# Kernel tuning notes

Measured on AMD Instinct MI355X. Metric: run time of the kernel, lower is better.

## Reference

```python
import jax, jax.numpy as jnp
import numpy as np

N = 50000
IN_CH = 128
OUT_CH = 64
H1, C1 = 8, 8


def gat_layer(x, src, dst, W, att_src, att_dst, bias, heads, out_ch, concat, n_nodes):
    # x: [N, F_in]; W: [F_in, heads*out_ch]; att_*: [heads, out_ch]; bias: [heads*out_ch] or [out_ch]
    h = (x @ W).reshape(n_nodes, heads, out_ch)              # [N,H,C]
    a_src = jnp.einsum('nhc,hc->nh', h, att_src)             # [N,H]
    a_dst = jnp.einsum('nhc,hc->nh', h, att_dst)             # [N,H]
    e = jax.nn.leaky_relu(a_src[src] + a_dst[dst], 0.2)      # [E,H]
    # segment softmax over incoming edges of each dst node
    m = jax.ops.segment_max(e, dst, num_segments=n_nodes)    # [N,H]
    p = jnp.exp(e - m[dst])                                  # [E,H]
    s = jax.ops.segment_sum(p, dst, num_segments=n_nodes)    # [N,H]
    alpha = p / (s[dst] + 1e-16)                             # [E,H]
    out = jax.ops.segment_sum(h[src] * alpha[:, :, None], dst, num_segments=n_nodes)  # [N,H,C]
    out = out.reshape(n_nodes, heads * out_ch) if concat else out.mean(axis=1)
    return out + bias


def setup_inputs() -> dict:
    key = jax.random.key(0)
    ks = jax.random.split(key, 12)
    E = 1600000
    x = jax.random.normal(ks[0], (N, IN_CH), dtype=jnp.float32)
    edge_index = jax.random.randint(ks[1], (2, E), 0, N, dtype=jnp.int64)
    sc = 0.1
    return {
        'x': x,
        'edge_index': edge_index,
        'W1': jax.random.normal(ks[2], (IN_CH, H1 * C1), dtype=jnp.float32) * sc,
        'att_src1': jax.random.normal(ks[3], (H1, C1), dtype=jnp.float32) * sc,
        'att_dst1': jax.random.normal(ks[4], (H1, C1), dtype=jnp.float32) * sc,
        'b1': jnp.zeros((H1 * C1,), dtype=jnp.float32),
        'W2': jax.random.normal(ks[5], (H1 * C1, OUT_CH), dtype=jnp.float32) * sc,
        'att_src2': jax.random.normal(ks[6], (1, OUT_CH), dtype=jnp.float32) * sc,
        'att_dst2': jax.random.normal(ks[7], (1, OUT_CH), dtype=jnp.float32) * sc,
        'b2': jnp.zeros((OUT_CH,), dtype=jnp.float32),
        'lin_W': jax.random.normal(ks[8], (OUT_CH, 1), dtype=jnp.float32) * sc,
        'lin_b': jnp.zeros((1,), dtype=jnp.float32),
    }


def reference(x, edge_index, W1, att_src1, att_dst1, b1, W2, att_src2, att_dst2, b2, lin_W, lin_b):
    # add self loops (PyG GATConv default)
    loops = jnp.arange(N, dtype=edge_index.dtype)
    src = jnp.concatenate([edge_index[0], loops])
    dst = jnp.concatenate([edge_index[1], loops])
    # dropout layers are identity in eval mode
    h = gat_layer(x, src, dst, W1, att_src1, att_dst1, b1, H1, C1, True, N)
    h = jax.nn.elu(h)
    h = gat_layer(h, src, dst, W2, att_src2, att_dst2, b2, 1, OUT_CH, False, N)
    return h @ lin_W + lin_b
```

## Files before the change

### kernel.cpp

```cpp
#include <hip/hip_runtime.h>
#include <hip/hip_bf16.h>
#include <math.h>

#define NN     50000
#define FIN    128
#define F1     64
#define NH1    8
#define F2     64

#define BSH    256
#define NB     ((NN + BSH - 1) / BSH)
#define BCAP   9472

typedef __bf16 bf16x8 __attribute__((ext_vector_type(8)));
typedef float  f32x4  __attribute__((ext_vector_type(4)));


__device__ __forceinline__ float loadF(const void* p, long long i, int fp32) {
    if (fp32) return ((const float*)p)[i];
    return __bfloat162float(((const __hip_bfloat16*)p)[i]);
}
__device__ __forceinline__ int loadI_nt(const void* p, long long i, int i64) {
    if (i64) return (int)__builtin_nontemporal_load(&((const long long*)p)[i]);
    return __builtin_nontemporal_load(&((const int*)p)[i]);
}
__device__ __forceinline__ unsigned short f2bfu(float f) {
    unsigned u = __float_as_uint(f);
    return (unsigned short)((u + 0x7FFFu + ((u >> 16) & 1u)) >> 16);
}
__device__ __forceinline__ float b2f(unsigned short u) {
    return __uint_as_float(((unsigned)u) << 16);
}


#define PREB 49

__global__ __launch_bounds__(256) void k_pre(
    const void* __restrict__ x, const void* __restrict__ ei,
    int* __restrict__ flags,
    const void* __restrict__ W1, const void* __restrict__ W2,
    unsigned short* __restrict__ W1p, unsigned short* __restrict__ W2p,
    int* __restrict__ bcnt) {
    __shared__ int s_nanexp, s_oddnz, s_fp32;
    if (threadIdx.x == 0) { s_nanexp = 0; s_oddnz = 0; }
    if (blockIdx.x == 0 && threadIdx.x < NB) bcnt[threadIdx.x] = 0;
    __syncthreads();
    const unsigned short* u = (const unsigned short*)x;
    int cnt = 0;
    for (int i = threadIdx.x; i < 8192; i += 256) {
        unsigned short v = u[i];
        if ((v & 0x7F80) == 0x7F80) cnt++;
    }
    if (cnt) atomicAdd(&s_nanexp, cnt);
    const unsigned* e32 = (const unsigned*)ei;
    int nz = 0;
    for (int i = threadIdx.x; i < 2048; i += 256) {
        if (e32[2 * i + 1] != 0u) nz++;
    }
    if (nz) atomicAdd(&s_oddnz, nz);
    __syncthreads();
    if (threadIdx.x == 0) {
        s_fp32 = (s_nanexp > 2) ? 1 : 0;
        if (blockIdx.x == 0) {
            flags[0] = s_fp32;
            flags[1] = (s_oddnz == 0) ? 1 : 0;
        }
    }
    __syncthreads();
    int fp32 = s_fp32;
    int gt = blockIdx.x * 256 + threadIdx.x, gs = PREB * 256;
    for (int i = gt; i < (FIN / 32) * 4 * 512; i += gs) {
        int j = i & 7, l = (i >> 3) & 63, f = i >> 9;
        int kb = f >> 2, nt = f & 3;
        int k = kb * 32 + (l >> 4) * 8 + j, n = nt * 16 + (l & 15);
        W1p[i] = f2bfu(loadF(W1, k * 64 + n, fp32));
    }
    for (int i = gt; i < (F1 / 32) * 4 * 512; i += gs) {
        int j = i & 7, l = (i >> 3) & 63, f = i >> 9;
        int kb = f >> 2, nt = f & 3;
        int k = kb * 32 + (l >> 4) * 8 + j, n = nt * 16 + (l & 15);
        W2p[i] = f2bfu(loadF(W2, k * 64 + n, fp32));
    }
}


__global__ __launch_bounds__(1024) void k_bin_fine(
    const void* __restrict__ ei, int E, int Etot,
    int* __restrict__ bcnt, unsigned* __restrict__ binned,
    const int* __restrict__ flags) {
    int i64 = flags[1];
    __shared__ int hist[NB], gbase[NB];
    for (int i = threadIdx.x; i < NB; i += 1024) hist[i] = 0;
    __syncthreads();
    long long base = (long long)blockIdx.x * 8192;
    unsigned pk[8]; short bb[8];
    #pragma unroll
    for (int u = 0; u < 8; ++u) {
        long long j = base + u * 1024 + threadIdx.x;
        int s = -1, d = -1;
        if (j < Etot) {
            if (j < E) { s = loadI_nt(ei, j, i64); d = loadI_nt(ei, (long long)E + j, i64); }
            else       { s = d = (int)(j - E); }
        }
        if ((unsigned)s < NN && (unsigned)d < NN) {
            bb[u] = (short)(d >> 8);
            pk[u] = ((unsigned)s << 8) | (unsigned)(d & 255);
            atomicAdd(&hist[bb[u]], 1);
        } else bb[u] = -1;
    }
    __syncthreads();
    for (int i = threadIdx.x; i < NB; i += 1024) {
        int h = hist[i];
        gbase[i] = h ? atomicAdd(&bcnt[i], h) : 0;
        hist[i] = 0;
    }
    __syncthreads();
    #pragma unroll
    for (int u = 0; u < 8; ++u) {
        if (bb[u] >= 0) {
            int pos = gbase[bb[u]] + atomicAdd(&hist[bb[u]], 1);
            if (pos < BCAP) binned[(size_t)bb[u] * BCAP + pos] = pk[u];
        }
    }
}

__global__ __launch_bounds__(1024) void k_csr_local(
    const int* __restrict__ bcnt, const unsigned* __restrict__ binned,
    int* __restrict__ offs, int* __restrict__ perm) {
    __shared__ int hist[BSH], cur[BSH], sd[BSH];
    int bk = blockIdx.x, tid = threadIdx.x;
    int n0 = bk * BSH;
    if (tid < 256) sd[tid] = (tid < NB) ? min(bcnt[tid], BCAP) : 0;
    __syncthreads();
    for (int off = 1; off < BSH; off <<= 1) {
        int t = 0;
        if (tid < 256 && tid >= off) t = sd[tid - off];
        __syncthreads();
        if (tid < 256) sd[tid] += t;
        __syncthreads();
    }
    int gb = (bk > 0) ? sd[bk - 1] : 0;
    if (bk == 0 && tid == 0) offs[NN] = sd[NB - 1];
    __syncthreads();
    int cnt = bcnt[bk]; if (cnt > BCAP) cnt = BCAP;
    const unsigned* bp = binned + (size_t)bk * BCAP;
    if (tid < 256) hist[tid] = 0;
    __syncthreads();
    for (int i = tid; i < cnt; i += 1024)
        atomicAdd(&hist[bp[i] & 255], 1);
    __syncthreads();
    int myh = (tid < 256) ? hist[tid] : 0;
    if (tid < 256) sd[tid] = myh;
    __syncthreads();
    for (int off = 1; off < BSH; off <<= 1) {
        int t = 0;
        if (tid < 256 && tid >= off) t = sd[tid - off];
        __syncthreads();
        if (tid < 256) sd[tid] += t;
        __syncthreads();
    }
    if (tid < 256) {
        int excl = sd[tid] - myh;
        cur[tid] = gb + excl;
        if (n0 + tid < NN) offs[n0 + tid] = gb + excl;
    }
    __syncthreads();
    for (int i = tid; i < cnt; i += 1024) {
        unsigned pk = bp[i];
        int pos = atomicAdd(&cur[pk & 255], 1);
        perm[pos] = (int)(pk >> 8);
    }
}


__global__ __launch_bounds__(256) void k_mgemm1(
    const void* __restrict__ x, const unsigned short* __restrict__ W1p,
    const void* __restrict__ attS, const void* __restrict__ attD,
    __hip_bfloat16* __restrict__ h1, float* __restrict__ a1s,
    float* __restrict__ a1d, const int* __restrict__ flags) {
    int fp32 = flags[0];
    __shared__ unsigned short hl[64 * 64];
    __shared__ float attSl[64], attDl[64];
    int tid = threadIdx.x;
    if (tid < 64) { attSl[tid] = loadF(attS, tid, fp32); attDl[tid] = loadF(attD, tid, fp32); }
    int w = tid >> 6, l = tid & 63;
    int quad = l >> 4, lm = l & 15;
    int n0 = blockIdx.x * 64;

    bf16x8 bfr[16];
    #pragma unroll
    for (int f = 0; f < 16; ++f)
        bfr[f] = *(const bf16x8*)(W1p + f * 512 + l * 8);

    int nodeA = n0 + w * 16 + lm;
    long long rowA = (nodeA < NN) ? nodeA : 0;
    f32x4 acc[4];
    #pragma unroll
    for (int nt = 0; nt < 4; ++nt) acc[nt] = (f32x4){0.f, 0.f, 0.f, 0.f};

    #pragma unroll
    for (int kb = 0; kb < 4; ++kb) {
        bf16x8 af;
        if (!fp32) {
            af = *(const bf16x8*)((const unsigned short*)x + rowA * FIN + kb * 32 + quad * 8);
        } else {
            const float* xf = (const float*)x + rowA * FIN + kb * 32 + quad * 8;
            union { unsigned short s[8]; bf16x8 v; } tmp;
            #pragma unroll
            for (int j = 0; j < 8; ++j) tmp.s[j] = f2bfu(xf[j]);
            af = tmp.v;
        }
        #pragma unroll
        for (int nt = 0; nt < 4; ++nt)
            acc[nt] = __builtin_amdgcn_mfma_f32_16x16x32_bf16(af, bfr[kb * 4 + nt], acc[nt], 0, 0, 0);
    }

    #pragma unroll
    for (int nt = 0; nt < 4; ++nt) {
        #pragma unroll
        for (int r = 0; r < 4; ++r) {
            int nl = w * 16 + quad * 4 + r;
            int node = n0 + nl;
            int c = nt * 16 + lm;
            unsigned short hb = f2bfu(acc[nt][r]);
            hl[nl * 64 + c] = hb;
            if (node < NN) ((unsigned short*)h1)[(size_t)node * 64 + c] = hb;
        }
    }
    __syncthreads();
    #pragma unroll
    for (int pp = 0; pp < 2; ++pp) {
        int p = tid + pp * 256;
        int nl = p >> 3, g = p & 7;
        int node = n0 + nl;
        float ss = 0.f, dd = 0.f;
        #pragma unroll
        for (int j = 0; j < 8; ++j) {
            float hv = b2f(hl[nl * 64 + g * 8 + j]);
            ss += hv * attSl[g * 8 + j];
            dd += hv * attDl[g * 8 + j];
        }
        if (node < NN) {
            a1s[(size_t)node * NH1 + g] = ss;
            a1d[(size_t)node * NH1 + g] = dd;
        }
    }
}


#define HLP 72

__global__ __launch_bounds__(256) void k_agg1f(
    const int* __restrict__ offs, const int* __restrict__ perm,
    const __hip_bfloat16* __restrict__ h1, const float* __restrict__ a1s,
    const float* __restrict__ a1d, const void* __restrict__ b1,
    const unsigned short* __restrict__ W2p,
    const void* __restrict__ attS2, const void* __restrict__ attD2,
    __hip_bfloat16* __restrict__ h2, float* __restrict__ a2s,
    float* __restrict__ a2d, int n, const int* __restrict__ flags) {
    int fp32 = flags[0];
    __shared__ unsigned short hl[16 * HLP];
    __shared__ float attSl[64], attDl[64];
    __shared__ float sp[16 * 4], dp[16 * 4];
    int tid = threadIdx.x;
    if (tid < 64) { attSl[tid] = loadF(attS2, tid, fp32); attDl[tid] = loadF(attD2, tid, fp32); }
    int w = tid >> 6, c = tid & 63;
    int n0 = blockIdx.x * 16;
    int u = c & 7, h = c >> 3, cb = c & 56;
    const unsigned short* hu = (const unsigned short*)h1;

    for (int m = 0; m < 4; ++m) {
        int d = n0 + w * 4 + m;
        if (d < n) {
            int start = offs[d], end = offs[d + 1];
            float adl = a1d[(size_t)d * NH1 + h];
            float acc = 0.f, denp = 0.f;
            for (int i = start; i < end; i += 8) {
                int j = i + u;
                int jc = (j < end) ? j : (end - 1);
                int sj = perm[jc];
                float e = a1s[(size_t)sj * NH1 + h] + adl;
                e = fmaxf(e, 0.2f * e);
                float p = (j < end) ? __expf(e) : 0.f;
                denp += p;
                #pragma unroll
                for (int k = 0; k < 8; ++k) {
                    int su = __builtin_amdgcn_readlane(sj, k);
                    float pk = __shfl(p, cb + k, 64);
                    acc = fmaf(pk, b2f(hu[(size_t)su * 64 + c]), acc);
                }
            }
            denp += __shfl_xor(denp, 1, 64);
            denp += __shfl_xor(denp, 2, 64);
            denp += __shfl_xor(denp, 4, 64);
            float v = acc / (denp + 1e-16f) + loadF(b1, c, fp32);
            v = (v > 0.f) ? v : expm1f(v);
            hl[(w * 4 + m) * HLP + c] = f2bfu(v);
        }
    }
    __syncthreads();

    int quad = c >> 4, lm = c & 15;
    bf16x8 bf0 = *(const bf16x8*)(W2p + (0 * 4 + w) * 512 + c * 8);
    bf16x8 bf1 = *(const bf16x8*)(W2p + (1 * 4 + w) * 512 + c * 8);
    bf16x8 af0 = *(const bf16x8*)(hl + lm * HLP + 0 * 32 + quad * 8);
    bf16x8 af1 = *(const bf16x8*)(hl + lm * HLP + 1 * 32 + quad * 8);
    f32x4 acc2 = (f32x4){0.f, 0.f, 0.f, 0.f};
    acc2 = __builtin_amdgcn_mfma_f32_16x16x32_bf16(af0, bf0, acc2, 0, 0, 0);
    acc2 = __builtin_amdgcn_mfma_f32_16x16x32_bf16(af1, bf1, acc2, 0, 0, 0);

    int cg = w * 16 + lm;
    float aSc = attSl[cg], aDc = attDl[cg];
    #pragma unroll
    for (int r = 0; r < 4; ++r) {
        int nl = quad * 4 + r;
        int node = n0 + nl;
        unsigned short hb = f2bfu(acc2[r]);
        if (node < n) ((unsigned short*)h2)[(size_t)node * 64 + cg] = hb;
        float hv = b2f(hb);
        float pvs = hv * aSc, pvd = hv * aDc;
        pvs += __shfl_xor(pvs, 1, 64); pvd += __shfl_xor(pvd, 1, 64);
        pvs += __shfl_xor(pvs, 2, 64); pvd += __shfl_xor(pvd, 2, 64);
        pvs += __shfl_xor(pvs, 4, 64); pvd += __shfl_xor(pvd, 4, 64);
        pvs += __shfl_xor(pvs, 8, 64); pvd += __shfl_xor(pvd, 8, 64);
        if (lm == 0) { sp[nl * 4 + w] = pvs; dp[nl * 4 + w] = pvd; }
    }
    __syncthreads();
    if (tid < 16) {
        int node = n0 + tid;
        if (node < n) {
            a2s[node] = sp[tid * 4 + 0] + sp[tid * 4 + 1] + sp[tid * 4 + 2] + sp[tid * 4 + 3];
            a2d[node] = dp[tid * 4 + 0] + dp[tid * 4 + 1] + dp[tid * 4 + 2] + dp[tid * 4 + 3];
        }
    }
}


__global__ __launch_bounds__(256) void k_agg2(
    const int* __restrict__ offs, const int* __restrict__ perm,
    const __hip_bfloat16* __restrict__ h2, const float* __restrict__ a2s,
    const float* __restrict__ a2d, const void* __restrict__ b2,
    const void* __restrict__ linW, const void* __restrict__ linb,
    void* __restrict__ out, int n, const int* __restrict__ flags) {
    int fp32 = flags[0];
    int w = threadIdx.x >> 6, c = threadIdx.x & 63;
    int d = blockIdx.x * 4 + w;
    if (d >= n) return;
    int start = offs[d], end = offs[d + 1];
    int u = c & 7;
    float ad = a2d[d];
    const unsigned short* hu = (const unsigned short*)h2;
    float acc = 0.f, denp = 0.f;
    for (int i = start; i < end; i += 8) {
        int j = i + u;
        int jc = (j < end) ? j : (end - 1);
        int sj = perm[jc];
        float e = a2s[sj] + ad;
        e = fmaxf(e, 0.2f * e);
        float p = (j < end) ? __expf(e) : 0.f;
        denp += (c < 8) ? p : 0.f;
        #pragma unroll
        for (int k = 0; k < 8; ++k) {
            int su = __builtin_amdgcn_readlane(sj, k);
            float pk = __uint_as_float(__builtin_amdgcn_readlane(__float_as_uint(p), k));
            acc = fmaf(pk, b2f(hu[(size_t)su * 64 + c]), acc);
        }
    }
    #pragma unroll
    for (int off = 1; off < 64; off <<= 1) denp += __shfl_xor(denp, off, 64);
    float v = acc / (denp + 1e-16f) + loadF(b2, c, fp32);
    float part = v * loadF(linW, c, fp32);
    #pragma unroll
    for (int off = 1; off < 64; off <<= 1) part += __shfl_xor(part, off, 64);
    if (c == 0) {
        float r = part + loadF(linb, 0, fp32);
        if (fp32) ((float*)out)[d] = r;
        else      ((__hip_bfloat16*)out)[d] = __float2bfloat16(r);
    }
}


static inline char* carve(char*& p, size_t bytes) {
    char* r = p;
    p += (bytes + 255) & ~size_t(255);
    return r;
}

extern "C" void kernel_launch(void* const* d_in, const int* in_sizes, int n_in,
                              void* d_out, int out_size, void* d_ws, size_t ws_size,
                              hipStream_t stream) {
    const void* x     = d_in[0];
    const void* ei    = d_in[1];
    const void* W1    = d_in[2];
    const void* attS1 = d_in[3];
    const void* attD1 = d_in[4];
    const void* b1    = d_in[5];
    const void* W2    = d_in[6];
    const void* attS2 = d_in[7];
    const void* attD2 = d_in[8];
    const void* b2    = d_in[9];
    const void* linW  = d_in[10];
    const void* linb  = d_in[11];

    int E    = in_sizes[1] / 2;
    int Etot = E + NN;

    char* p = (char*)d_ws;
    int*   flags = (int*)carve(p, 256);
    int*   bcnt  = (int*)carve(p, (size_t)NB * 4);
    unsigned short* W1p = (unsigned short*)carve(p, 8192 * 2);
    unsigned short* W2p = (unsigned short*)carve(p, 4096 * 2);
    int*   offs  = (int*)carve(p, (size_t)(NN + 1) * 4);
    int*   perm  = (int*)carve(p, (size_t)Etot * 4);
    char*  big   = carve(p, 9600000);
    unsigned* binned = (unsigned*)big;
    float*    a1s    = (float*)big;
    float*    a1d    = (float*)(big + 1600000);
    __hip_bfloat16* h1 = (__hip_bfloat16*)(big + 3200000);
    __hip_bfloat16* h2  = (__hip_bfloat16*)carve(p, (size_t)NN * F2 * 2);
    float* a2s = (float*)carve(p, (size_t)NN * 4);
    float* a2d = (float*)carve(p, (size_t)NN * 4);

    k_pre<<<PREB, 256, 0, stream>>>(x, ei, flags, W1, W2, W1p, W2p, bcnt);

    int ab = (Etot + 8191) / 8192;
    k_bin_fine<<<ab, 1024, 0, stream>>>(ei, E, Etot, bcnt, binned, flags);
    k_csr_local<<<NB, 1024, 0, stream>>>(bcnt, binned, offs, perm);

    int ng = (NN + 63) / 64;
    k_mgemm1<<<ng, 256, 0, stream>>>(x, W1p, attS1, attD1, h1, a1s, a1d, flags);
    k_agg1f<<<(NN + 15) / 16, 256, 0, stream>>>(offs, perm, h1, a1s, a1d, b1,
                                                W2p, attS2, attD2, h2, a2s, a2d, NN, flags);
    k_agg2<<<(NN + 3) / 4, 256, 0, stream>>>(offs, perm, h2, a2s, a2d, b2, linW, linb, d_out, NN, flags);
}
```

Measured before the change: 232.8 us.

## Merge independent front-end kernels into combined launches to overlap preprocessing

Fuses weight packing with edge binning into one launch, and CSR construction with the first GEMM into another. Block ranges are split by blockIdx, so independent work runs concurrently and two launches plus their gaps go away. Binning blocks now work out the index width themselves, and bcnt is cleared with a memset. Because the first GEMM now runs alongside CSR building, binned can no longer share storage with h1/a1s, which raises workspace use. The GEMM blocks are also enlarged to 1024 threads, which may change occupancy.

```diff
diff --git a/kernel.cpp b/kernel.cpp
--- a/kernel.cpp
+++ b/kernel.cpp
@@ -11,6 +11,8 @@
 #define BSH    256
 #define NB     ((NN + BSH - 1) / BSH)
 #define BCAP   9472
+#define PREB   13
+#define MG1B   ((NN + 255) / 256)
 
 typedef __bf16 bf16x8 __attribute__((ext_vector_type(8)));
 typedef float  f32x4  __attribute__((ext_vector_type(4)));
@@ -33,216 +35,220 @@
 }
 
 
-#define PREB 49
-
-__global__ __launch_bounds__(256) void k_pre(
-    const void* __restrict__ x, const void* __restrict__ ei,
+__global__ __launch_bounds__(1024) void k_front(
+    const void* __restrict__ x, const void* __restrict__ ei, int E, int Etot,
     int* __restrict__ flags,
     const void* __restrict__ W1, const void* __restrict__ W2,
     unsigned short* __restrict__ W1p, unsigned short* __restrict__ W2p,
-    int* __restrict__ bcnt) {
-    __shared__ int s_nanexp, s_oddnz, s_fp32;
-    if (threadIdx.x == 0) { s_nanexp = 0; s_oddnz = 0; }
-    if (blockIdx.x == 0 && threadIdx.x < NB) bcnt[threadIdx.x] = 0;
-    __syncthreads();
-    const unsigned short* u = (const unsigned short*)x;
-    int cnt = 0;
-    for (int i = threadIdx.x; i < 8192; i += 256) {
-        unsigned short v = u[i];
-        if ((v & 0x7F80) == 0x7F80) cnt++;
-    }
-    if (cnt) atomicAdd(&s_nanexp, cnt);
-    const unsigned* e32 = (const unsigned*)ei;
-    int nz = 0;
-    for (int i = threadIdx.x; i < 2048; i += 256) {
-        if (e32[2 * i + 1] != 0u) nz++;
-    }
-    if (nz) atomicAdd(&s_oddnz, nz);
-    __syncthreads();
-    if (threadIdx.x == 0) {
-        s_fp32 = (s_nanexp > 2) ? 1 : 0;
-        if (blockIdx.x == 0) {
-            flags[0] = s_fp32;
-            flags[1] = (s_oddnz == 0) ? 1 : 0;
-        }
-    }
-    __syncthreads();
-    int fp32 = s_fp32;
-    int gt = blockIdx.x * 256 + threadIdx.x, gs = PREB * 256;
-    for (int i = gt; i < (FIN / 32) * 4 * 512; i += gs) {
-        int j = i & 7, l = (i >> 3) & 63, f = i >> 9;
-        int kb = f >> 2, nt = f & 3;
-        int k = kb * 32 + (l >> 4) * 8 + j, n = nt * 16 + (l & 15);
-        W1p[i] = f2bfu(loadF(W1, k * 64 + n, fp32));
-    }
-    for (int i = gt; i < (F1 / 32) * 4 * 512; i += gs) {
-        int j = i & 7, l = (i >> 3) & 63, f = i >> 9;
-        int kb = f >> 2, nt = f & 3;
-        int k = kb * 32 + (l >> 4) * 8 + j, n = nt * 16 + (l & 15);
-        W2p[i] = f2bfu(loadF(W2, k * 64 + n, fp32));
-    }
-}
-
-
-__global__ __launch_bounds__(1024) void k_bin_fine(
-    const void* __restrict__ ei, int E, int Etot,
-    int* __restrict__ bcnt, unsigned* __restrict__ binned,
-    const int* __restrict__ flags) {
-    int i64 = flags[1];
+    int* __restrict__ bcnt, unsigned* __restrict__ binned) {
+    __shared__ int s_a, s_b;
     __shared__ int hist[NB], gbase[NB];
-    for (int i = threadIdx.x; i < NB; i += 1024) hist[i] = 0;
-    __syncthreads();
-    long long base = (long long)blockIdx.x * 8192;
-    unsigned pk[8]; short bb[8];
-    #pragma unroll
-    for (int u = 0; u < 8; ++u) {
-        long long j = base + u * 1024 + threadIdx.x;
-        int s = -1, d = -1;
-        if (j < Etot) {
-            if (j < E) { s = loadI_nt(ei, j, i64); d = loadI_nt(ei, (long long)E + j, i64); }
-            else       { s = d = (int)(j - E); }
-        }
-        if ((unsigned)s < NN && (unsigned)d < NN) {
-            bb[u] = (short)(d >> 8);
-            pk[u] = ((unsigned)s << 8) | (unsigned)(d & 255);
-            atomicAdd(&hist[bb[u]], 1);
-        } else bb[u] = -1;
-    }
-    __syncthreads();
-    for (int i = threadIdx.x; i < NB; i += 1024) {
-        int h = hist[i];
-        gbase[i] = h ? atomicAdd(&bcnt[i], h) : 0;
-        hist[i] = 0;
-    }
-    __syncthreads();
-    #pragma unroll
-    for (int u = 0; u < 8; ++u) {
-        if (bb[u] >= 0) {
-            int pos = gbase[bb[u]] + atomicAdd(&hist[bb[u]], 1);
-            if (pos < BCAP) binned[(size_t)bb[u] * BCAP + pos] = pk[u];
-        }
-    }
-}
-
-__global__ __launch_bounds__(1024) void k_csr_local(
+    int tid = threadIdx.x;
+    if (blockIdx.x < PREB) {
+        if (tid == 0) { s_a = 0; s_b = 0; }
+        __syncthreads();
+        const unsigned short* u = (const unsigned short*)x;
+        int cnt = 0;
+        for (int i = tid; i < 8192; i += 1024) {
+            unsigned short v = u[i];
+            if ((v & 0x7F80) == 0x7F80) cnt++;
+        }
+        if (cnt) atomicAdd(&s_a, cnt);
+        const unsigned* e32 = (const unsigned*)ei;
+        int nz = 0;
+        for (int i = tid; i < 2048; i += 1024) {
+            if (e32[2 * i + 1] != 0u) nz++;
+        }
+        if (nz) atomicAdd(&s_b, nz);
+        __syncthreads();
+        int fp32 = (s_a > 2) ? 1 : 0;
+        if (tid == 0 && blockIdx.x == 0) {
+            flags[0] = fp32;
+            flags[1] = (s_b == 0) ? 1 : 0;
+        }
+        int gt = blockIdx.x * 1024 + tid, gs = PREB * 1024;
+        for (int i = gt; i < (FIN / 32) * 4 * 512; i += gs) {
+            int j = i & 7, l = (i >> 3) & 63, f = i >> 9;
+            int kb = f >> 2, nt = f & 3;
+            int k = kb * 32 + (l >> 4) * 8 + j, n = nt * 16 + (l & 15);
+            W1p[i] = f2bfu(loadF(W1, k * 64 + n, fp32));
+        }
+        for (int i = gt; i < (F1 / 32) * 4 * 512; i += gs) {
+            int j = i & 7, l = (i >> 3) & 63, f = i >> 9;
+            int kb = f >> 2, nt = f & 3;
+            int k = kb * 32 + (l >> 4) * 8 + j, n = nt * 16 + (l & 15);
+            W2p[i] = f2bfu(loadF(W2, k * 64 + n, fp32));
+        }
+    } else {
+        if (tid == 0) s_b = 0;
+        for (int i = tid; i < NB; i += 1024) hist[i] = 0;
+        __syncthreads();
+        const unsigned* e32 = (const unsigned*)ei;
+        int nz = 0;
+        for (int i = tid; i < 2048; i += 1024) {
+            if (e32[2 * i + 1] != 0u) nz++;
+        }
+        if (nz) atomicAdd(&s_b, nz);
+        __syncthreads();
+        int i64 = (s_b == 0) ? 1 : 0;
+        long long base = (long long)(blockIdx.x - PREB) * 8192;
+        unsigned pk[8]; short bb[8];
+        #pragma unroll
+        for (int u = 0; u < 8; ++u) {
+            long long j = base + u * 1024 + tid;
+            int s = -1, d = -1;
+            if (j < Etot) {
+                if (j < E) { s = loadI_nt(ei, j, i64); d = loadI_nt(ei, (long long)E + j, i64); }
+                else       { s = d = (int)(j - E); }
+            }
+            if ((unsigned)s < NN && (unsigned)d < NN) {
+                bb[u] = (short)(d >> 8);
+                pk[u] = ((unsigned)s << 8) | (unsigned)(d & 255);
+                atomicAdd(&hist[bb[u]], 1);
+            } else bb[u] = -1;
+        }
+        __syncthreads();
+        for (int i = tid; i < NB; i += 1024) {
+            int h = hist[i];
+            gbase[i] = h ? atomicAdd(&bcnt[i], h) : 0;
+            hist[i] = 0;
+        }
+        __syncthreads();
+        #pragma unroll
+        for (int u = 0; u < 8; ++u) {
+            if (bb[u] >= 0) {
+                int pos = gbase[bb[u]] + atomicAdd(&hist[bb[u]], 1);
+                if (pos < BCAP) binned[(size_t)bb[u] * BCAP + pos] = pk[u];
+            }
+        }
+    }
+}
+
+
+__global__ __launch_bounds__(1024) void k_mid(
     const int* __restrict__ bcnt, const unsigned* __restrict__ binned,
-    int* __restrict__ offs, int* __restrict__ perm) {
-    __shared__ int hist[BSH], cur[BSH], sd[BSH];
-    int bk = blockIdx.x, tid = threadIdx.x;
-    int n0 = bk * BSH;
-    if (tid < 256) sd[tid] = (tid < NB) ? min(bcnt[tid], BCAP) : 0;
-    __syncthreads();
-    for (int off = 1; off < BSH; off <<= 1) {
-        int t = 0;
-        if (tid < 256 && tid >= off) t = sd[tid - off];
-        __syncthreads();
-        if (tid < 256) sd[tid] += t;
-        __syncthreads();
-    }
-    int gb = (bk > 0) ? sd[bk - 1] : 0;
-    if (bk == 0 && tid == 0) offs[NN] = sd[NB - 1];
-    __syncthreads();
-    int cnt = bcnt[bk]; if (cnt > BCAP) cnt = BCAP;
-    const unsigned* bp = binned + (size_t)bk * BCAP;
-    if (tid < 256) hist[tid] = 0;
-    __syncthreads();
-    for (int i = tid; i < cnt; i += 1024)
-        atomicAdd(&hist[bp[i] & 255], 1);
-    __syncthreads();
-    int myh = (tid < 256) ? hist[tid] : 0;
-    if (tid < 256) sd[tid] = myh;
-    __syncthreads();
-    for (int off = 1; off < BSH; off <<= 1) {
-        int t = 0;
-        if (tid < 256 && tid >= off) t = sd[tid - off];
-        __syncthreads();
-        if (tid < 256) sd[tid] += t;
-        __syncthreads();
-    }
-    if (tid < 256) {
-        int excl = sd[tid] - myh;
-        cur[tid] = gb + excl;
-        if (n0 + tid < NN) offs[n0 + tid] = gb + excl;
-    }
-    __syncthreads();
-    for (int i = tid; i < cnt; i += 1024) {
-        unsigned pk = bp[i];
-        int pos = atomicAdd(&cur[pk & 255], 1);
-        perm[pos] = (int)(pk >> 8);
-    }
-}
-
-
-__global__ __launch_bounds__(256) void k_mgemm1(
+    int* __restrict__ offs, int* __restrict__ perm,
     const void* __restrict__ x, const unsigned short* __restrict__ W1p,
     const void* __restrict__ attS, const void* __restrict__ attD,
     __hip_bfloat16* __restrict__ h1, float* __restrict__ a1s,
     float* __restrict__ a1d, const int* __restrict__ flags) {
-    int fp32 = flags[0];
-    __shared__ unsigned short hl[64 * 64];
-    __shared__ float attSl[64], attDl[64];
+    __shared__ __align__(16) char smem[33280];
     int tid = threadIdx.x;
-    if (tid < 64) { attSl[tid] = loadF(attS, tid, fp32); attDl[tid] = loadF(attD, tid, fp32); }
-    int w = tid >> 6, l = tid & 63;
-    int quad = l >> 4, lm = l & 15;
-    int n0 = blockIdx.x * 64;
-
-    bf16x8 bfr[16];
-    #pragma unroll
-    for (int f = 0; f < 16; ++f)
-        bfr[f] = *(const bf16x8*)(W1p + f * 512 + l * 8);
-
-    int nodeA = n0 + w * 16 + lm;
-    long long rowA = (nodeA < NN) ? nodeA : 0;
-    f32x4 acc[4];
-    #pragma unroll
-    for (int nt = 0; nt < 4; ++nt) acc[nt] = (f32x4){0.f, 0.f, 0.f, 0.f};
-
-    #pragma unroll
-    for (int kb = 0; kb < 4; ++kb) {
-        bf16x8 af;
-        if (!fp32) {
-            af = *(const bf16x8*)((const unsigned short*)x + rowA * FIN + kb * 32 + quad * 8);
-        } else {
-            const float* xf = (const float*)x + rowA * FIN + kb * 32 + quad * 8;
-            union { unsigned short s[8]; bf16x8 v; } tmp;
+    if (blockIdx.x < NB) {
+        int* hist = (int*)smem;
+        int* cur  = (int*)(smem + 1024);
+        int* sd   = (int*)(smem + 2048);
+        int bk = blockIdx.x;
+        int n0 = bk * BSH;
+        if (tid < 256) sd[tid] = (tid < NB) ? min(bcnt[tid], BCAP) : 0;
+        __syncthreads();
+        for (int off = 1; off < BSH; off <<= 1) {
+            int t = 0;
+            if (tid < 256 && tid >= off) t = sd[tid - off];
+            __syncthreads();
+            if (tid < 256) sd[tid] += t;
+            __syncthreads();
+        }
+        int gb = (bk > 0) ? sd[bk - 1] : 0;
+        if (bk == 0 && tid == 0) offs[NN] = sd[NB - 1];
+        __syncthreads();
+        int cnt = bcnt[bk]; if (cnt > BCAP) cnt = BCAP;
+        const unsigned* bp = binned + (size_t)bk * BCAP;
+        if (tid < 256) hist[tid] = 0;
+        __syncthreads();
+        for (int i = tid; i < cnt; i += 1024)
+            atomicAdd(&hist[bp[i] & 255], 1);
+        __syncthreads();
+        int myh = (tid < 256) ? hist[tid] : 0;
+        if (tid < 256) sd[tid] = myh;
+        __syncthreads();
+        for (int off = 1; off < BSH; off <<= 1) {
+            int t = 0;
+            if (tid < 256 && tid >= off) t = sd[tid - off];
+            __syncthreads();
+            if (tid < 256) sd[tid] += t;
+            __syncthreads();
+        }
+        if (tid < 256) {
+            int excl = sd[tid] - myh;
+            cur[tid] = gb + excl;
+            if (n0 + tid < NN) offs[n0 + tid] = gb + excl;
+        }
+        __syncthreads();
+        for (int i = tid; i < cnt; i += 1024) {
+            unsigned pk = bp[i];
+            int pos = atomicAdd(&cur[pk & 255], 1);
+            perm[pos] = (int)(pk >> 8);
+        }
+    } else {
+        int fp32 = flags[0];
+        unsigned short* hl = (unsigned short*)smem;
+        float* attSl = (float*)(smem + 32768);
+        float* attDl = (float*)(smem + 32768 + 256);
+        if (tid < 64) { attSl[tid] = loadF(attS, tid, fp32); attDl[tid] = loadF(attD, tid, fp32); }
+        int sub = tid >> 8, t = tid & 255;
+        int w = t >> 6, l = t & 63;
+        int quad = l >> 4, lm = l & 15;
+        int n0 = (blockIdx.x - NB) * 256 + sub * 64;
+        unsigned short* hls = hl + sub * 4096;
+
+        bf16x8 bfr[16];
+        #pragma unroll
+        for (int f = 0; f < 16; ++f)
+            bfr[f] = *(const bf16x8*)(W1p + f * 512 + l * 8);
+
+        int nodeA = n0 + w * 16 + lm;
+        long long rowA = (nodeA < NN) ? nodeA : 0;
+        f32x4 acc[4];
+        #pragma unroll
+        for (int nt = 0; nt < 4; ++nt) acc[nt] = (f32x4){0.f, 0.f, 0.f, 0.f};
+
+        #pragma unroll
+        for (int kb = 0; kb < 4; ++kb) {
+            bf16x8 af;
+            if (!fp32) {
+                af = *(const bf16x8*)((const unsigned short*)x + rowA * FIN + kb * 32 + quad * 8);
+            } else {
+                const float* xf = (const float*)x + rowA * FIN + kb * 32 + quad * 8;
+                union { unsigned short s[8]; bf16x8 v; } tmp;
+                #pragma unroll
+                for (int j = 0; j < 8; ++j) tmp.s[j] = f2bfu(xf[j]);
+                af = tmp.v;
+            }
             #pragma unroll
-            for (int j = 0; j < 8; ++j) tmp.s[j] = f2bfu(xf[j]);
-            af = tmp.v;
-        }
-        #pragma unroll
-        for (int nt = 0; nt < 4; ++nt)
-            acc[nt] = __builtin_amdgcn_mfma_f32_16x16x32_bf16(af, bfr[kb * 4 + nt], acc[nt], 0, 0, 0);
-    }
-
-    #pragma unroll
-    for (int nt = 0; nt < 4; ++nt) {
-        #pragma unroll
-        for (int r = 0; r < 4; ++r) {
-            int nl = w * 16 + quad * 4 + r;
+            for (int nt = 0; nt < 4; ++nt)
+                acc[nt] = __builtin_amdgcn_mfma_f32_16x16x32_bf16(af, bfr[kb * 4 + nt], acc[nt], 0, 0, 0);
+        }
+
+        #pragma unroll
+        for (int nt = 0; nt < 4; ++nt) {
+            #pragma unroll
+            for (int r = 0; r < 4; ++r) {
+                int nl = w * 16 + quad * 4 + r;
+                int node = n0 + nl;
+                int c = nt * 16 + lm;
+                unsigned short hb = f2bfu(acc[nt][r]);
+                hls[nl * 64 + c] = hb;
+                if (node < NN) ((unsigned short*)h1)[(size_t)node * 64 + c] = hb;
+            }
+        }
+        __syncthreads();
+        #pragma unroll
+        for (int pp = 0; pp < 2; ++pp) {
+            int p = t + pp * 256;
+            int nl = p >> 3, g = p & 7;
             int node = n0 + nl;
-            int c = nt * 16 + lm;
-            unsigned short hb = f2bfu(acc[nt][r]);
-            hl[nl * 64 + c] = hb;
-            if (node < NN) ((unsigned short*)h1)[(size_t)node * 64 + c] = hb;
-        }
-    }
-    __syncthreads();
-    #pragma unroll
-    for (int pp = 0; pp < 2; ++pp) {
-        int p = tid + pp * 256;
-        int nl = p >> 3, g = p & 7;
-        int node = n0 + nl;
-        float ss = 0.f, dd = 0.f;
-        #pragma unroll
-        for (int j = 0; j < 8; ++j) {
-            float hv = b2f(hl[nl * 64 + g * 8 + j]);
-            ss += hv * attSl[g * 8 + j];
-            dd += hv * attDl[g * 8 + j];
-        }
-        if (node < NN) {
-            a1s[(size_t)node * NH1 + g] = ss;
-            a1d[(size_t)node * NH1 + g] = dd;
+            float ss = 0.f, dd = 0.f;
+            #pragma unroll
+            for (int j = 0; j < 8; ++j) {
+                float hv = b2f(hls[nl * 64 + g * 8 + j]);
+                ss += hv * attSl[g * 8 + j];
+                dd += hv * attDl[g * 8 + j];
+            }
+            if (node < NN) {
+                a1s[(size_t)node * NH1 + g] = ss;
+                a1d[(size_t)node * NH1 + g] = dd;
+            }
         }
     }
 }
@@ -412,23 +418,21 @@
     unsigned short* W2p = (unsigned short*)carve(p, 4096 * 2);
     int*   offs  = (int*)carve(p, (size_t)(NN + 1) * 4);
     int*   perm  = (int*)carve(p, (size_t)Etot * 4);
-    char*  big   = carve(p, 9600000);
-    unsigned* binned = (unsigned*)big;
-    float*    a1s    = (float*)big;
-    float*    a1d    = (float*)(big + 1600000);
-    __hip_bfloat16* h1 = (__hip_bfloat16*)(big + 3200000);
-    __hip_bfloat16* h2  = (__hip_bfloat16*)carve(p, (size_t)NN * F2 * 2);
+    unsigned* binned = (unsigned*)carve(p, (size_t)NB * BCAP * 4);
+    float*    a1s    = (float*)carve(p, (size_t)NN * NH1 * 4);
+    float*    a1d    = (float*)carve(p, (size_t)NN * NH1 * 4);
+    __hip_bfloat16* h1 = (__hip_bfloat16*)carve(p, (size_t)NN * F1 * 2);
+    __hip_bfloat16* h2 = (__hip_bfloat16*)carve(p, (size_t)NN * F2 * 2);
     float* a2s = (float*)carve(p, (size_t)NN * 4);
     float* a2d = (float*)carve(p, (size_t)NN * 4);
 
-    k_pre<<<PREB, 256, 0, stream>>>(x, ei, flags, W1, W2, W1p, W2p, bcnt);
-
-    int ab = (Etot + 8191) / 8192;
-    k_bin_fine<<<ab, 1024, 0, stream>>>(ei, E, Etot, bcnt, binned, flags);
-    k_csr_local<<<NB, 1024, 0, stream>>>(bcnt, binned, offs, perm);
-
-    int ng = (NN + 63) / 64;
-    k_mgemm1<<<ng, 256, 0, stream>>>(x, W1p, attS1, attD1, h1, a1s, a1d, flags);
+    hipMemsetAsync(bcnt, 0, (size_t)NB * 4, stream);
+
+    int nbin = (Etot + 8191) / 8192;
+    k_front<<<PREB + nbin, 1024, 0, stream>>>(x, ei, E, Etot, flags,
+                                              W1, W2, W1p, W2p, bcnt, binned);
+    k_mid<<<NB + MG1B, 1024, 0, stream>>>(bcnt, binned, offs, perm,
+                                          x, W1p, attS1, attD1, h1, a1s, a1d, flags);
     k_agg1f<<<(NN + 15) / 16, 256, 0, stream>>>(offs, perm, h1, a1s, a1d, b1,
                                                 W2p, attS2, attD2, h2, a2s, a2d, NN, flags);
     k_agg2<<<(NN + 3) / 4, 256, 0, stream>>>(offs, perm, h2, a2s, a2d, b2, linW, linb, d_out, NN, flags);
```

Measured after the change: 225.0 us. -3.4%, faster.
